# Kernel optimization log

Hardware: AMD Instinct MI355X
Metric: run time of the kernel (lower is better)

## Reference

```python
import jax, jax.numpy as jnp
import numpy as np

N_NODES = 100000
N_EDGES = 1600000
FEAT = 128
HID = 128
CLASSES = 10
GRAPHS = 64


def gcn_conv(x, W, b, src, dst, n):
    # PyG GCNConv: h = x @ W; add self-loops; symmetric deg^{-1/2} norm; scatter-add; + bias
    h = x @ W
    src_f = jnp.concatenate([src, jnp.arange(n, dtype=src.dtype)])
    dst_f = jnp.concatenate([dst, jnp.arange(n, dtype=dst.dtype)])
    deg = jax.ops.segment_sum(jnp.ones_like(dst_f, dtype=h.dtype), dst_f, num_segments=n)
    dinv = jax.lax.rsqrt(jnp.where(deg > 0, deg, 1.0))
    norm = dinv[src_f] * dinv[dst_f]              # [E+N]
    msg = h[src_f] * norm[:, None]                # gather + scale
    out = jax.ops.segment_sum(msg, dst_f, num_segments=n)  # scatter-add
    return out + b


def global_mean_pool(x, batch, num_graphs):
    s = jax.ops.segment_sum(x, batch, num_segments=num_graphs)
    cnt = jax.ops.segment_sum(jnp.ones_like(batch, dtype=x.dtype), batch, num_segments=num_graphs)
    return s / jnp.maximum(cnt, 1.0)[:, None]


def setup_inputs() -> dict:
    key = jax.random.key(0)
    ks = jax.random.split(key, 10)
    x = jax.random.normal(ks[0], (N_NODES, FEAT), dtype=jnp.float32)
    edge_index = jax.random.randint(ks[1], (2, N_EDGES), 0, N_NODES, dtype=jnp.int64)
    batch = jnp.sort(jax.random.randint(ks[2], (N_NODES,), 0, GRAPHS, dtype=jnp.int64))
    def glorot(k, fi, fo):
        s = float(np.sqrt(6.0 / (fi + fo)))
        return jax.random.uniform(k, (fi, fo), jnp.float32, -s, s)
    return {
        "x": x, "edge_index": edge_index, "batch": batch,
        "W1": glorot(ks[3], FEAT, HID), "b1": jnp.zeros((HID,), jnp.float32),
        "W2": glorot(ks[4], HID, HID), "b2": jnp.zeros((HID,), jnp.float32),
        "W3": glorot(ks[5], HID, HID), "b3": jnp.zeros((HID,), jnp.float32),
        "Wlin": glorot(ks[6], HID, CLASSES), "blin": jnp.zeros((CLASSES,), jnp.float32),
    }


def reference(x, edge_index, batch, W1, b1, W2, b2, W3, b3, Wlin, blin):
    src, dst = edge_index[0], edge_index[1]
    n = x.shape[0]
    h = jax.nn.relu(gcn_conv(x, W1, b1, src, dst, n))
    h = jax.nn.relu(gcn_conv(h, W2, b2, src, dst, n))
    h = gcn_conv(h, W3, b3, src, dst, n)
    emb = global_mean_pool(h, batch, GRAPHS)      # [GRAPHS, HID]
    # dropout(p=0.5) is identity in eval mode
    logits = emb @ Wlin + blin                    # [GRAPHS, CLASSES]
    return logits, jnp.squeeze(emb)
```

## Files before the change

### kernel.cpp

```cpp
#include <hip/hip_runtime.h>
#include <hip/hip_bf16.h>
#include <stdint.h>

typedef unsigned int uint32;
typedef __attribute__((ext_vector_type(8))) short short8;
typedef __attribute__((ext_vector_type(4))) float float4v;

#define FEAT 128
#define NGRAPH 64
#define GB   256
#define NBK  512

__device__ __forceinline__ float bf2f_lo(uint32 v) {
    union { uint32 i; float f; } u; u.i = v << 16; return u.f;
}
__device__ __forceinline__ float bf2f_hi(uint32 v) {
    union { uint32 i; float f; } u; u.i = v & 0xffff0000u; return u.f;
}
__device__ __forceinline__ unsigned short f2bf(float f) {
    uint32 u = __builtin_bit_cast(uint32, f);
    uint32 r = (u + 0x7fffu + ((u >> 16) & 1u)) >> 16;
    return (unsigned short)r;
}
__device__ __forceinline__ uint32 f2bf2(float lo, float hi) {
    return (uint32)f2bf(lo) | ((uint32)f2bf(hi) << 16);
}

__global__ void k_bhist(const int* __restrict__ dst, int* __restrict__ bhistT, int E) {
    __shared__ int h[NBK];
    int t = threadIdx.x, blk = blockIdx.x;
    for (int b = t; b < NBK; b += 256) h[b] = 0;
    __syncthreads();
    int chunk = (E + GB - 1) / GB;
    int lo = blk * chunk, hi = min(lo + chunk, E);
    for (int e = lo + t; e < hi; e += 256)
        atomicAdd(&h[dst[e] >> 8], 1);
    __syncthreads();
    for (int b = t; b < NBK; b += 256) bhistT[b * GB + blk] = h[b];
}

__global__ void k_boffs(int* __restrict__ bhistT, int* __restrict__ bbase) {
    __shared__ int sc[NBK];
    int t = threadIdx.x;
    int tot = 0;
#pragma unroll 8
    for (int blk = 0; blk < GB; blk++) {
        int v = bhistT[t * GB + blk];
        bhistT[t * GB + blk] = tot;
        tot += v;
    }
    sc[t] = tot;
    __syncthreads();
    for (int off = 1; off < NBK; off <<= 1) {
        int v = (t >= off) ? sc[t - off] : 0;
        __syncthreads();
        sc[t] += v;
        __syncthreads();
    }
    bbase[t] = sc[t] - tot;
    if (t == NBK - 1) bbase[NBK] = sc[t];
}

__global__ void k_bscat(const int* __restrict__ src, const int* __restrict__ dst,
                        const int* __restrict__ bhistT, const int* __restrict__ bbase,
                        uint32* __restrict__ ebuf, int E) {
    __shared__ int cur[NBK];
    int t = threadIdx.x, blk = blockIdx.x;
    for (int b = t; b < NBK; b += 256) cur[b] = bbase[b] + bhistT[b * GB + blk];
    __syncthreads();
    int chunk = (E + GB - 1) / GB;
    int lo = blk * chunk, hi = min(lo + chunk, E);
    for (int e = lo + t; e < hi; e += 256) {
        int d = dst[e], s = src[e];
        int b = d >> 8;
        int p = atomicAdd(&cur[b], 1);
        ebuf[p] = ((uint32)s << 8) | (uint32)(d & 255);
    }
}

__global__ void k_csr(const uint32* __restrict__ ebuf, const int* __restrict__ bbase,
                      float* __restrict__ dinv, int* __restrict__ rowp,
                      int* __restrict__ csrc, int N, int E) {
    __shared__ int h[256];
    __shared__ int cur[256];
    int t = threadIdx.x, b = blockIdx.x;
    h[t] = 0;
    __syncthreads();
    int e0 = bbase[b], e1 = bbase[b + 1];
    for (int e = e0 + t; e < e1; e += 256)
        atomicAdd(&h[ebuf[e] & 255u], 1);
    __syncthreads();
    int deg = h[t];
    cur[t] = deg;
    __syncthreads();
    for (int off = 1; off < 256; off <<= 1) {
        int v = (t >= off) ? cur[t - off] : 0;
        __syncthreads();
        cur[t] += v;
        __syncthreads();
    }
    int r = bbase[b] + cur[t] - deg;
    int node = b * 256 + t;
    if (node < N) {
        rowp[node] = r;
        dinv[node] = rsqrtf((float)deg + 1.0f);
    }
    if (b == 0 && t == 0) rowp[N] = E;
    cur[t] = r;
    __syncthreads();
    for (int e = e0 + t; e < e1; e += 256) {
        uint32 v = ebuf[e];
        int p = atomicAdd(&cur[v & 255u], 1);
        csrc[p] = (int)(v >> 8);
    }
}

__global__ void k_wswz3(const float* __restrict__ W1, const float* __restrict__ W2,
                        const float* __restrict__ W3, unsigned short* __restrict__ o1,
                        unsigned short* __restrict__ o2, unsigned short* __restrict__ o3) {
    int wid = blockIdx.x >> 3;
    const float* W = (wid == 0) ? W1 : (wid == 1) ? W2 : W3;
    unsigned short* out = (wid == 0) ? o1 : (wid == 1) ? o2 : o3;
    int e = (blockIdx.x & 7) * 256 + threadIdx.x;
    int kt = e >> 9, ct = (e >> 6) & 7, lane = e & 63;
    int krow = kt * 32 + (lane >> 4) * 8;
    int col = ct * 16 + (lane & 15);
#pragma unroll
    for (int j = 0; j < 8; j++)
        out[e * 8 + j] = f2bf(W[(krow + j) * FEAT + col]);
}

template <bool F32IN>
__global__ void k_gemm(const void* __restrict__ Xp,
                       const unsigned short* __restrict__ Wswz,
                       const float* __restrict__ dinv,
                       unsigned short* __restrict__ Hb, int N) {
    __shared__ unsigned short Wl[FEAT * FEAT];
    {
        const uint4* Wg = (const uint4*)Wswz;
        uint4* Ws = (uint4*)Wl;
        for (int i = threadIdx.x; i < 2048; i += 256) Ws[i] = Wg[i];
    }
    __syncthreads();

    int wave = threadIdx.x >> 6, lane = threadIdx.x & 63;
    int r0 = (blockIdx.x * 4 + wave) * 16;
    if (r0 >= N) return;
    int m = lane & 15, q = lane >> 4;

    int arow = r0 + m; if (arow >= N) arow = N - 1;
    short8 a[4];
    if (F32IN) {
        const float* Ar = (const float*)Xp + (long)arow * FEAT;
#pragma unroll
        for (int kt = 0; kt < 4; kt++) {
            float4 u = *(const float4*)(Ar + kt * 32 + q * 8);
            float4 v = *(const float4*)(Ar + kt * 32 + q * 8 + 4);
            short8 tv;
            tv[0] = (short)f2bf(u.x); tv[1] = (short)f2bf(u.y);
            tv[2] = (short)f2bf(u.z); tv[3] = (short)f2bf(u.w);
            tv[4] = (short)f2bf(v.x); tv[5] = (short)f2bf(v.y);
            tv[6] = (short)f2bf(v.z); tv[7] = (short)f2bf(v.w);
            a[kt] = tv;
        }
    } else {
        const short8* Ar = (const short8*)((const unsigned short*)Xp + (long)arow * FEAT);
#pragma unroll
        for (int kt = 0; kt < 4; kt++) a[kt] = Ar[kt * 4 + q];
    }

    const short8* Bl = (const short8*)Wl;
    float4v acc[8];
#pragma unroll
    for (int ct = 0; ct < 8; ct++) acc[ct] = (float4v){0.f, 0.f, 0.f, 0.f};
#pragma unroll
    for (int ct = 0; ct < 8; ct++) {
        acc[ct] = __builtin_amdgcn_mfma_f32_16x16x32_bf16(a[0], Bl[(0 * 8 + ct) * 64 + lane], acc[ct], 0, 0, 0);
        acc[ct] = __builtin_amdgcn_mfma_f32_16x16x32_bf16(a[1], Bl[(1 * 8 + ct) * 64 + lane], acc[ct], 0, 0, 0);
        acc[ct] = __builtin_amdgcn_mfma_f32_16x16x32_bf16(a[2], Bl[(2 * 8 + ct) * 64 + lane], acc[ct], 0, 0, 0);
        acc[ct] = __builtin_amdgcn_mfma_f32_16x16x32_bf16(a[3], Bl[(3 * 8 + ct) * 64 + lane], acc[ct], 0, 0, 0);
    }

    float ds[4];
#pragma unroll
    for (int reg = 0; reg < 4; reg++) {
        int row = r0 + q * 4 + reg;
        ds[reg] = (row < N) ? dinv[row] : 0.f;
    }
#pragma unroll
    for (int ct = 0; ct < 8; ct++) {
#pragma unroll
        for (int reg = 0; reg < 4; reg++) {
            int row = r0 + q * 4 + reg;
            if (row < N) Hb[(long)row * FEAT + ct * 16 + m] = f2bf(acc[ct][reg] * ds[reg]);
        }
    }
}

__global__ void k_agg(const uint32* __restrict__ Hb,
                      const int* __restrict__ rowp, const int* __restrict__ csrc,
                      const float* __restrict__ dinv, const float* __restrict__ bias,
                      uint32* __restrict__ OUTb, int N, int relu) {
    int wave = threadIdx.x >> 6, lane = threadIdx.x & 63;
    int i = blockIdx.x * 4 + wave;
    if (i >= N) return;
    int f = lane & 31, half = lane >> 5;
    const uint2* H2 = (const uint2*)Hb;
    float a0 = 0.f, a1 = 0.f, a2 = 0.f, a3 = 0.f;
    int e0 = rowp[i], e1 = rowp[i + 1];
    int e = e0;
    for (; e + 16 <= e1; e += 16) {
        int  s[8];
        uint2 h[8];
#pragma unroll
        for (int j = 0; j < 8; j++) s[j] = csrc[e + 2 * j + half];
#pragma unroll
        for (int j = 0; j < 8; j++) h[j] = H2[(long)s[j] * 32 + f];
#pragma unroll
        for (int j = 0; j < 8; j++) {
            a0 += bf2f_lo(h[j].x); a1 += bf2f_hi(h[j].x);
            a2 += bf2f_lo(h[j].y); a3 += bf2f_hi(h[j].y);
        }
    }
    {
        int r = e1 - e;
        int  s[8];
        uint2 h[8];
#pragma unroll
        for (int j = 0; j < 8; j++) {
            int idx = 2 * j + half;
            if (idx < r) s[j] = csrc[e + idx];
        }
#pragma unroll
        for (int j = 0; j < 8; j++)
            if (2 * j + half < r) h[j] = H2[(long)s[j] * 32 + f];
#pragma unroll
        for (int j = 0; j < 8; j++)
            if (2 * j + half < r) {
                a0 += bf2f_lo(h[j].x); a1 += bf2f_hi(h[j].x);
                a2 += bf2f_lo(h[j].y); a3 += bf2f_hi(h[j].y);
            }
    }
    a0 += __shfl_xor(a0, 32);
    a1 += __shfl_xor(a1, 32);
    a2 += __shfl_xor(a2, 32);
    a3 += __shfl_xor(a3, 32);
    if (half == 0) {
        uint2 hv = H2[(long)i * 32 + f];
        a0 += bf2f_lo(hv.x); a1 += bf2f_hi(hv.x);
        a2 += bf2f_lo(hv.y); a3 += bf2f_hi(hv.y);
        float di = dinv[i];
        float4 bb = ((const float4*)bias)[f];
        a0 = a0 * di + bb.x; a1 = a1 * di + bb.y;
        a2 = a2 * di + bb.z; a3 = a3 * di + bb.w;
        if (relu) {
            a0 = fmaxf(a0, 0.f); a1 = fmaxf(a1, 0.f);
            a2 = fmaxf(a2, 0.f); a3 = fmaxf(a3, 0.f);
        }
        uint2 o;
        o.x = f2bf2(a0, a1);
        o.y = f2bf2(a2, a3);
        ((uint2*)OUTb)[(long)i * 32 + f] = o;
    }
}

__global__ void k_pool(const uint32* __restrict__ Gb, const int* __restrict__ batch,
                       float* __restrict__ pool, int* __restrict__ cntg, int N) {
    int t = threadIdx.x;
    int nb = gridDim.x;
    int chunk = (N + nb - 1) / nb;
    int lo = blockIdx.x * chunk, hi = min(lo + chunk, N);
    if (lo >= hi) return;
    float ax = 0.f, ay = 0.f;
    int cnt = 0;
    int cg = batch[lo];
    for (int i = lo; i < hi; i++) {
        int g = batch[i];
        if (g != cg) {
            atomicAdd(&pool[cg * FEAT + 2 * t], ax);
            atomicAdd(&pool[cg * FEAT + 2 * t + 1], ay);
            if (t == 0) atomicAdd(&cntg[cg], cnt);
            ax = ay = 0.f; cnt = 0; cg = g;
        }
        uint32 v = Gb[(long)i * 64 + t];
        ax += bf2f_lo(v); ay += bf2f_hi(v);
        cnt++;
    }
    atomicAdd(&pool[cg * FEAT + 2 * t], ax);
    atomicAdd(&pool[cg * FEAT + 2 * t + 1], ay);
    if (t == 0) atomicAdd(&cntg[cg], cnt);
}

__global__ void k_final(const float* __restrict__ pool, const int* __restrict__ cntg,
                        const float* __restrict__ Wlin, const float* __restrict__ blin,
                        float* __restrict__ out) {
    __shared__ float es[FEAT];
    int g = blockIdx.x, t = threadIdx.x;
    float c = (float)max(cntg[g], 1);
    float e = pool[g * FEAT + t] / c;
    es[t] = e;
    out[NGRAPH * 10 + g * FEAT + t] = e;
    __syncthreads();
    if (t < 10) {
        float a = blin[t];
        for (int k = 0; k < FEAT; k++)
            a += es[k] * Wlin[k * 10 + t];
        out[g * 10 + t] = a;
    }
}

extern "C" void kernel_launch(void* const* d_in, const int* in_sizes, int n_in,
                              void* d_out, int out_size, void* d_ws, size_t ws_size,
                              hipStream_t stream) {
    const float* x    = (const float*)d_in[0];
    const int*   ei   = (const int*)d_in[1];
    const int*   batch= (const int*)d_in[2];
    const float* W1   = (const float*)d_in[3];
    const float* b1   = (const float*)d_in[4];
    const float* W2   = (const float*)d_in[5];
    const float* b2   = (const float*)d_in[6];
    const float* W3   = (const float*)d_in[7];
    const float* b3   = (const float*)d_in[8];
    const float* Wlin = (const float*)d_in[9];
    const float* blin = (const float*)d_in[10];

    const int N = in_sizes[2];
    const int E = in_sizes[1] / 2;
    const int* src = ei;
    const int* dst = ei + E;
    const int NB = (N + 255) >> 8;

    char* w = (char*)d_ws;
    auto take = [&](size_t bytes) {
        char* p = w;
        w += (bytes + 255) & ~(size_t)255;
        return p;
    };
    float*  dinv   = (float*) take((size_t)N * 4);
    int*    rowp   = (int*)   take((size_t)(N + 1) * 4);
    int*    csrc   = (int*)   take((size_t)E * 4);
    uint32* ebuf   = (uint32*)take((size_t)E * 4);
    int*    bhistT = (int*)   take((size_t)GB * NBK * 4);
    int*    bbase  = (int*)   take((size_t)(NBK + 1) * 4);
    uint32* hbuf   = (uint32*)take((size_t)N * FEAT * 2);
    uint32* gbuf   = (uint32*)take((size_t)N * FEAT * 2);
    unsigned short* w1s = (unsigned short*)take(FEAT * FEAT * 2);
    unsigned short* w2s = (unsigned short*)take(FEAT * FEAT * 2);
    unsigned short* w3s = (unsigned short*)take(FEAT * FEAT * 2);
    float*  pool   = (float*) take((size_t)NGRAPH * FEAT * 4);
    int*    cntg   = (int*)   take((size_t)NGRAPH * 4);
    (void)ws_size; (void)n_in; (void)out_size;

    hipMemsetAsync(pool, 0, (size_t)NGRAPH * FEAT * 4, stream);
    hipMemsetAsync(cntg, 0, (size_t)NGRAPH * 4, stream);

    k_bhist<<<GB, 256, 0, stream>>>(dst, bhistT, E);
    k_boffs<<<1, NBK, 0, stream>>>(bhistT, bbase);
    k_bscat<<<GB, 256, 0, stream>>>(src, dst, bhistT, bbase, ebuf, E);
    k_csr  <<<NB, 256, 0, stream>>>(ebuf, bbase, dinv, rowp, csrc, N, E);

    k_wswz3<<<24, 256, 0, stream>>>(W1, W2, W3, w1s, w2s, w3s);

    const int tile_blocks = (N + 63) / 64;
    const int agg_blocks  = (N + 3) / 4;

    k_gemm<true> <<<tile_blocks, 256, 0, stream>>>(x, w1s, dinv, (unsigned short*)hbuf, N);
    k_agg<<<agg_blocks, 256, 0, stream>>>(hbuf, rowp, csrc, dinv, b1, gbuf, N, 1);
    k_gemm<false><<<tile_blocks, 256, 0, stream>>>(gbuf, w2s, dinv, (unsigned short*)hbuf, N);
    k_agg<<<agg_blocks, 256, 0, stream>>>(hbuf, rowp, csrc, dinv, b2, gbuf, N, 1);
    k_gemm<false><<<tile_blocks, 256, 0, stream>>>(gbuf, w3s, dinv, (unsigned short*)hbuf, N);
    k_agg<<<agg_blocks, 256, 0, stream>>>(hbuf, rowp, csrc, dinv, b3, gbuf, N, 0);

    k_pool <<<1024, 64, 0, stream>>>(gbuf, batch, pool, cntg, N);
    k_final<<<NGRAPH, 128, 0, stream>>>(pool, cntg, Wlin, blin, (float*)d_out);
}
```

Before: 483.7 us.

## Fuse final aggregation with mean pooling, parallelize bucket offset scan, drop memsets

```diff
diff --git a/kernel.cpp b/kernel.cpp
--- a/kernel.cpp
+++ b/kernel.cpp
@@ -26,9 +26,14 @@
     return (uint32)f2bf(lo) | ((uint32)f2bf(hi) << 16);
 }
 
-__global__ void k_bhist(const int* __restrict__ dst, int* __restrict__ bhistT, int E) {
+__global__ void k_bhist(const int* __restrict__ dst, int* __restrict__ bhistT,
+                        float* __restrict__ pool, int* __restrict__ cntg, int E) {
     __shared__ int h[NBK];
     int t = threadIdx.x, blk = blockIdx.x;
+    if (blk == 0) {
+        for (int i = t; i < NGRAPH * FEAT; i += 256) pool[i] = 0.f;
+        if (t < NGRAPH) cntg[t] = 0;
+    }
     for (int b = t; b < NBK; b += 256) h[b] = 0;
     __syncthreads();
     int chunk = (E + GB - 1) / GB;
@@ -39,17 +44,30 @@
     for (int b = t; b < NBK; b += 256) bhistT[b * GB + blk] = h[b];
 }
 
-__global__ void k_boffs(int* __restrict__ bhistT, int* __restrict__ bbase) {
+__global__ void k_boffs_a(int* __restrict__ bhistT, int* __restrict__ btot) {
+    int b = blockIdx.x, l = threadIdx.x;
+    int v[4];
+    int base = b * GB + l * 4;
+#pragma unroll
+    for (int j = 0; j < 4; j++) v[j] = bhistT[base + j];
+    int s = v[0] + v[1] + v[2] + v[3];
+    int incl = s;
+    for (int off = 1; off < 64; off <<= 1) {
+        int u = __shfl_up(incl, off);
+        if (l >= off) incl += u;
+    }
+    int excl = incl - s;
+    int p0 = excl, p1 = p0 + v[0], p2 = p1 + v[1], p3 = p2 + v[2];
+    bhistT[base + 0] = p0; bhistT[base + 1] = p1;
+    bhistT[base + 2] = p2; bhistT[base + 3] = p3;
+    if (l == 63) btot[b] = incl;
+}
+
+__global__ void k_boffs_b(const int* __restrict__ btot, int* __restrict__ bbase) {
     __shared__ int sc[NBK];
     int t = threadIdx.x;
-    int tot = 0;
-#pragma unroll 8
-    for (int blk = 0; blk < GB; blk++) {
-        int v = bhistT[t * GB + blk];
-        bhistT[t * GB + blk] = tot;
-        tot += v;
-    }
-    sc[t] = tot;
+    int s = btot[t];
+    sc[t] = s;
     __syncthreads();
     for (int off = 1; off < NBK; off <<= 1) {
         int v = (t >= off) ? sc[t - off] : 0;
@@ -57,7 +75,7 @@
         sc[t] += v;
         __syncthreads();
     }
-    bbase[t] = sc[t] - tot;
+    bbase[t] = sc[t] - s;
     if (t == NBK - 1) bbase[NBK] = sc[t];
 }
 
@@ -200,7 +218,7 @@
 __global__ void k_agg(const uint32* __restrict__ Hb,
                       const int* __restrict__ rowp, const int* __restrict__ csrc,
                       const float* __restrict__ dinv, const float* __restrict__ bias,
-                      uint32* __restrict__ OUTb, int N, int relu) {
+                      uint32* __restrict__ OUTb, int N) {
     int wave = threadIdx.x >> 6, lane = threadIdx.x & 63;
     int i = blockIdx.x * 4 + wave;
     if (i >= N) return;
@@ -251,12 +269,10 @@
         a2 += bf2f_lo(hv.y); a3 += bf2f_hi(hv.y);
         float di = dinv[i];
         float4 bb = ((const float4*)bias)[f];
-        a0 = a0 * di + bb.x; a1 = a1 * di + bb.y;
-        a2 = a2 * di + bb.z; a3 = a3 * di + bb.w;
-        if (relu) {
-            a0 = fmaxf(a0, 0.f); a1 = fmaxf(a1, 0.f);
-            a2 = fmaxf(a2, 0.f); a3 = fmaxf(a3, 0.f);
-        }
+        a0 = fmaxf(a0 * di + bb.x, 0.f);
+        a1 = fmaxf(a1 * di + bb.y, 0.f);
+        a2 = fmaxf(a2 * di + bb.z, 0.f);
+        a3 = fmaxf(a3 * di + bb.w, 0.f);
         uint2 o;
         o.x = f2bf2(a0, a1);
         o.y = f2bf2(a2, a3);
@@ -264,31 +280,102 @@
     }
 }
 
-__global__ void k_pool(const uint32* __restrict__ Gb, const int* __restrict__ batch,
-                       float* __restrict__ pool, int* __restrict__ cntg, int N) {
+__global__ void k_aggpool(const uint32* __restrict__ Hb,
+                          const int* __restrict__ rowp, const int* __restrict__ csrc,
+                          const float* __restrict__ dinv, const float* __restrict__ bias,
+                          const int* __restrict__ batch,
+                          float* __restrict__ pool, int* __restrict__ cntg, int N) {
+    __shared__ float rows[4][FEAT];
+    __shared__ int gid[4];
+    int wave = threadIdx.x >> 6, lane = threadIdx.x & 63;
+    int i = blockIdx.x * 4 + wave;
+    int f = lane & 31, half = lane >> 5;
+    if (i < N) {
+        const uint2* H2 = (const uint2*)Hb;
+        float a0 = 0.f, a1 = 0.f, a2 = 0.f, a3 = 0.f;
+        int e0 = rowp[i], e1 = rowp[i + 1];
+        int e = e0;
+        for (; e + 16 <= e1; e += 16) {
+            int  s[8];
+            uint2 h[8];
+#pragma unroll
+            for (int j = 0; j < 8; j++) s[j] = csrc[e + 2 * j + half];
+#pragma unroll
+            for (int j = 0; j < 8; j++) h[j] = H2[(long)s[j] * 32 + f];
+#pragma unroll
+            for (int j = 0; j < 8; j++) {
+                a0 += bf2f_lo(h[j].x); a1 += bf2f_hi(h[j].x);
+                a2 += bf2f_lo(h[j].y); a3 += bf2f_hi(h[j].y);
+            }
+        }
+        {
+            int r = e1 - e;
+            int  s[8];
+            uint2 h[8];
+#pragma unroll
+            for (int j = 0; j < 8; j++) {
+                int idx = 2 * j + half;
+                if (idx < r) s[j] = csrc[e + idx];
+            }
+#pragma unroll
+            for (int j = 0; j < 8; j++)
+                if (2 * j + half < r) h[j] = H2[(long)s[j] * 32 + f];
+#pragma unroll
+            for (int j = 0; j < 8; j++)
+                if (2 * j + half < r) {
+                    a0 += bf2f_lo(h[j].x); a1 += bf2f_hi(h[j].x);
+                    a2 += bf2f_lo(h[j].y); a3 += bf2f_hi(h[j].y);
+                }
+        }
+        a0 += __shfl_xor(a0, 32);
+        a1 += __shfl_xor(a1, 32);
+        a2 += __shfl_xor(a2, 32);
+        a3 += __shfl_xor(a3, 32);
+        if (half == 0) {
+            const uint2* H2b = (const uint2*)Hb;
+            uint2 hv = H2b[(long)i * 32 + f];
+            a0 += bf2f_lo(hv.x); a1 += bf2f_hi(hv.x);
+            a2 += bf2f_lo(hv.y); a3 += bf2f_hi(hv.y);
+            float di = dinv[i];
+            float4 bb = ((const float4*)bias)[f];
+            rows[wave][4 * f + 0] = a0 * di + bb.x;
+            rows[wave][4 * f + 1] = a1 * di + bb.y;
+            rows[wave][4 * f + 2] = a2 * di + bb.z;
+            rows[wave][4 * f + 3] = a3 * di + bb.w;
+            if (lane == 0) gid[wave] = batch[i];
+        }
+    } else if (lane == 0) {
+        gid[wave] = -1;
+    }
+    __syncthreads();
     int t = threadIdx.x;
-    int nb = gridDim.x;
-    int chunk = (N + nb - 1) / nb;
-    int lo = blockIdx.x * chunk, hi = min(lo + chunk, N);
-    if (lo >= hi) return;
-    float ax = 0.f, ay = 0.f;
-    int cnt = 0;
-    int cg = batch[lo];
-    for (int i = lo; i < hi; i++) {
-        int g = batch[i];
-        if (g != cg) {
-            atomicAdd(&pool[cg * FEAT + 2 * t], ax);
-            atomicAdd(&pool[cg * FEAT + 2 * t + 1], ay);
-            if (t == 0) atomicAdd(&cntg[cg], cnt);
-            ax = ay = 0.f; cnt = 0; cg = g;
-        }
-        uint32 v = Gb[(long)i * 64 + t];
-        ax += bf2f_lo(v); ay += bf2f_hi(v);
-        cnt++;
-    }
-    atomicAdd(&pool[cg * FEAT + 2 * t], ax);
-    atomicAdd(&pool[cg * FEAT + 2 * t + 1], ay);
-    if (t == 0) atomicAdd(&cntg[cg], cnt);
+    if (t < FEAT) {
+        float s = 0.f;
+        int cg = -1;
+        for (int wv = 0; wv < 4; wv++) {
+            int g = gid[wv];
+            if (g < 0) break;
+            if (g != cg) {
+                if (cg >= 0) atomicAdd(&pool[cg * FEAT + t], s);
+                s = 0.f; cg = g;
+            }
+            s += rows[wv][t];
+        }
+        if (cg >= 0) atomicAdd(&pool[cg * FEAT + t], s);
+    } else if (t == FEAT) {
+        int cnt = 0;
+        int cg = -1;
+        for (int wv = 0; wv < 4; wv++) {
+            int g = gid[wv];
+            if (g < 0) break;
+            if (g != cg) {
+                if (cg >= 0) atomicAdd(&cntg[cg], cnt);
+                cnt = 0; cg = g;
+            }
+            cnt++;
+        }
+        if (cg >= 0) atomicAdd(&cntg[cg], cnt);
+    }
 }
 
 __global__ void k_final(const float* __restrict__ pool, const int* __restrict__ cntg,
@@ -341,6 +428,7 @@
     int*    csrc   = (int*)   take((size_t)E * 4);
     uint32* ebuf   = (uint32*)take((size_t)E * 4);
     int*    bhistT = (int*)   take((size_t)GB * NBK * 4);
+    int*    btot   = (int*)   take((size_t)NBK * 4);
     int*    bbase  = (int*)   take((size_t)(NBK + 1) * 4);
     uint32* hbuf   = (uint32*)take((size_t)N * FEAT * 2);
     uint32* gbuf   = (uint32*)take((size_t)N * FEAT * 2);
@@ -351,13 +439,11 @@
     int*    cntg   = (int*)   take((size_t)NGRAPH * 4);
     (void)ws_size; (void)n_in; (void)out_size;
 
-    hipMemsetAsync(pool, 0, (size_t)NGRAPH * FEAT * 4, stream);
-    hipMemsetAsync(cntg, 0, (size_t)NGRAPH * 4, stream);
-
-    k_bhist<<<GB, 256, 0, stream>>>(dst, bhistT, E);
-    k_boffs<<<1, NBK, 0, stream>>>(bhistT, bbase);
-    k_bscat<<<GB, 256, 0, stream>>>(src, dst, bhistT, bbase, ebuf, E);
-    k_csr  <<<NB, 256, 0, stream>>>(ebuf, bbase, dinv, rowp, csrc, N, E);
+    k_bhist  <<<GB, 256, 0, stream>>>(dst, bhistT, pool, cntg, E);
+    k_boffs_a<<<NBK, 64, 0, stream>>>(bhistT, btot);
+    k_boffs_b<<<1, NBK, 0, stream>>>(btot, bbase);
+    k_bscat  <<<GB, 256, 0, stream>>>(src, dst, bhistT, bbase, ebuf, E);
+    k_csr    <<<NB, 256, 0, stream>>>(ebuf, bbase, dinv, rowp, csrc, N, E);
 
     k_wswz3<<<24, 256, 0, stream>>>(W1, W2, W3, w1s, w2s, w3s);
 
@@ -365,12 +451,12 @@
     const int agg_blocks  = (N + 3) / 4;
 
     k_gemm<true> <<<tile_blocks, 256, 0, stream>>>(x, w1s, dinv, (unsigned short*)hbuf, N);
-    k_agg<<<agg_blocks, 256, 0, stream>>>(hbuf, rowp, csrc, dinv, b1, gbuf, N, 1);
+    k_agg<<<agg_blocks, 256, 0, stream>>>(hbuf, rowp, csrc, dinv, b1, gbuf, N);
     k_gemm<false><<<tile_blocks, 256, 0, stream>>>(gbuf, w2s, dinv, (unsigned short*)hbuf, N);
-    k_agg<<<agg_blocks, 256, 0, stream>>>(hbuf, rowp, csrc, dinv, b2, gbuf, N, 1);
+    k_agg<<<agg_blocks, 256, 0, stream>>>(hbuf, rowp, csrc, dinv, b2, gbuf, N);
     k_gemm<false><<<tile_blocks, 256, 0, stream>>>(gbuf, w3s, dinv, (unsigned short*)hbuf, N);
-    k_agg<<<agg_blocks, 256, 0, stream>>>(hbuf, rowp, csrc, dinv, b3, gbuf, N, 0);
-
-    k_pool <<<1024, 64, 0, stream>>>(gbuf, batch, pool, cntg, N);
+    k_aggpool<<<agg_blocks, 256, 0, stream>>>(hbuf, rowp, csrc, dinv, b3, batch,
+                                              pool, cntg, N);
+
     k_final<<<NGRAPH, 128, 0, stream>>>(pool, cntg, Wlin, blin, (float*)d_out);
 }
```

Measured after the change: 553.0 us. 14.3% more time.
